# Optimization experiments

Hardware: AMD Instinct MI355X
Metric: run time of the kernel (lower is better)

Reference implementation:

```python
import jax, jax.numpy as jnp
import numpy as np

VAR0, VAR1 = 0.1, 0.2
THRESH = 0.5
NEG_POS = 3
NEG_INF = -1e30


def point_form(b):
    # (cx,cy,w,h) -> (x1,y1,x2,y2)
    return jnp.concatenate([b[..., :2] - b[..., 2:] * 0.5,
                            b[..., :2] + b[..., 2:] * 0.5], -1)


def iou(a, b):
    # a: [G,4], b: [A,4], both xyxy -> [G,A]
    tl = jnp.maximum(a[:, None, :2], b[None, :, :2])
    br = jnp.minimum(a[:, None, 2:], b[None, :, 2:])
    wh = jnp.clip(br - tl, 0.0)
    inter = wh[..., 0] * wh[..., 1]
    area_a = (a[:, 2] - a[:, 0]) * (a[:, 3] - a[:, 1])
    area_b = (b[:, 2] - b[:, 0]) * (b[:, 3] - b[:, 1])
    return inter / (area_a[:, None] + area_b[None, :] - inter)


def encode_single(gt_boxes, gt_labels, anchors):
    # gt_boxes [G,4] xyxy, gt_labels [G], anchors [A,4] cxcywh
    ov = iou(gt_boxes, point_form(anchors))            # [G,A]
    best_prior_idx = jnp.argmax(ov, axis=1)            # [G] guaranteed match
    best_truth_ov = jnp.max(ov, axis=0)                # [A]
    best_truth_idx = jnp.argmax(ov, axis=0)            # [A]
    G = gt_boxes.shape[0]
    best_truth_ov = best_truth_ov.at[best_prior_idx].set(2.0)
    best_truth_idx = best_truth_idx.at[best_prior_idx].set(jnp.arange(G))
    matches = gt_boxes[best_truth_idx]                 # [A,4]
    conf = jnp.where(best_truth_ov < THRESH, 0, gt_labels[best_truth_idx] + 1)
    m_cxcy = (matches[:, :2] + matches[:, 2:]) * 0.5
    m_wh = matches[:, 2:] - matches[:, :2]
    g_cxcy = (m_cxcy - anchors[:, :2]) / (VAR0 * anchors[:, 2:])
    g_wh = jnp.log(m_wh / anchors[:, 2:]) / VAR1
    return conf, jnp.concatenate([g_cxcy, g_wh], -1)


def smooth_l1(d):
    ad = jnp.abs(d)
    return jnp.where(ad < 1.0, 0.5 * d * d, ad - 0.5)


def ssd_guarantee_loss(pred_conf, pred_loc, anchors_b, gt_boxes, gt_labels):
    # anchors_b: per-image anchors [B,A,4] (cxcywh)
    conf_t, loc_t = jax.vmap(encode_single)(gt_boxes, gt_labels, anchors_b)
    loc_t = jax.lax.stop_gradient(loc_t)               # loc_t.detach() in torch
    pos = conf_t > 0                                   # [B,A]
    N = jnp.sum(pos).astype(pred_loc.dtype)
    loc_loss = jnp.sum(jnp.where(pos[..., None], smooth_l1(pred_loc - loc_t), 0.0))
    logp = jax.nn.log_softmax(pred_conf, axis=-1)
    ce = -jnp.take_along_axis(logp, conf_t[..., None], axis=-1)[..., 0]  # [B,A]
    A = pred_conf.shape[1]
    pos_num = jnp.sum(pos, axis=1)                     # [B]
    neg_num = jnp.maximum(10, jnp.minimum(pos_num * NEG_POS, A - pos_num))
    neg_ce = jnp.where(conf_t == 0, ce, NEG_INF)
    neg_sorted = -jnp.sort(-neg_ce, axis=1)            # descending hard-negative sort
    rank = jnp.arange(A)
    take = (rank[None, :] < neg_num[:, None]) & (neg_sorted > 0.5 * NEG_INF)
    class_loss = (jnp.sum(jnp.where(pos, ce, 0.0))
                  + jnp.sum(jnp.where(take, neg_sorted, 0.0))) / N
    return class_loss, loc_loss / N, N


def decode(loc, anchors):
    # loc [B,A,4], anchors [A,4] cxcywh -> refined anchors [B,A,4] cxcywh
    cxcy = anchors[None, :, :2] + loc[..., :2] * VAR0 * anchors[None, :, 2:]
    wh = anchors[None, :, 2:] * jnp.exp(loc[..., 2:] * VAR1)
    return jnp.concatenate([cxcy, wh], -1)


def setup_inputs() -> dict:
    key = jax.random.key(0)
    ks = jax.random.split(key, 10)
    B, A, C, G = 32, 16320, 81, 32
    objectness = jax.random.normal(ks[0], (B, A, 2), jnp.float32)
    refine_loc = 0.1 * jax.random.normal(ks[1], (B, A, 4), jnp.float32)
    pred_conf = jax.random.normal(ks[2], (B, A, C), jnp.float32)
    pred_loc = 0.1 * jax.random.normal(ks[3], (B, A, 4), jnp.float32)
    # anchors: valid normalized cxcywh
    a_cxcy = 0.05 + 0.9 * jax.random.uniform(ks[4], (1, A, 2), jnp.float32)
    a_wh = 0.02 + 0.23 * jax.random.uniform(ks[5], (1, A, 2), jnp.float32)
    anchors = jnp.concatenate([a_cxcy, a_wh], -1)
    # gt boxes: valid xyxy in [0,1]
    g_cxcy = 0.2 + 0.6 * jax.random.uniform(ks[6], (B, G, 2), jnp.float32)
    g_wh = 0.05 + 0.25 * jax.random.uniform(ks[7], (B, G, 2), jnp.float32)
    gt_boxes = jnp.clip(jnp.concatenate([g_cxcy - g_wh * 0.5, g_cxcy + g_wh * 0.5], -1), 0.0, 1.0)
    gt_labels = jax.random.randint(ks[8], (B, G), 0, C - 1, jnp.int32)
    return {"objectness": objectness, "refine_loc": refine_loc, "pred_conf": pred_conf,
            "pred_loc": pred_loc, "anchors": anchors, "gt_boxes": gt_boxes,
            "gt_labels": gt_labels}


def reference(objectness, refine_loc, pred_conf, pred_loc, anchors, gt_boxes, gt_labels):
    a0 = anchors[0]                                    # [A,4]
    B = pred_conf.shape[0]
    anchors_b = jnp.broadcast_to(a0, (B,) + a0.shape)
    # ARM: binary objectness, labels zeroed
    arm_cls, arm_loc, _ = ssd_guarantee_loss(objectness, refine_loc, anchors_b,
                                             gt_boxes, jnp.zeros_like(gt_labels))
    # ODM: match against per-image refined anchors
    refined = decode(refine_loc, a0)
    odm_cls, odm_loc, _ = ssd_guarantee_loss(pred_conf, pred_loc, refined,
                                             gt_boxes, gt_labels)
    total = arm_cls + arm_loc + odm_cls + odm_loc
    return (total, odm_cls, odm_loc, arm_cls, arm_loc)
```

## Files before the change

### kernel.cpp

```cpp
#include <hip/hip_runtime.h>
#include <hip/hip_bf16.h>

constexpr int NB = 32;
constexpr int NA = 16320;
constexpr int NG = 32;
constexpr int NC = 81;
constexpr int ODM_GRID = 2048;

__device__ __forceinline__ float sl1(float d) {
    float ad = fabsf(d);
    return ad < 1.f ? 0.5f * d * d : ad - 0.5f;
}

__device__ __forceinline__ unsigned long long umax64(unsigned long long a, unsigned long long b) {
    return a > b ? a : b;
}

__global__ __launch_bounds__(256) void k_match(
    const float* __restrict__ anchors,
    const float* __restrict__ refine_loc,
    const float* __restrict__ gt_boxes,
    float* __restrict__ ws_ov,
    unsigned char* __restrict__ ws_idx,
    unsigned long long* __restrict__ ws_part)
{
    int row = blockIdx.x >> 6;
    int chunk = blockIdx.x & 63;
    int lossId = row >> 5, b = row & 31;
    int tid = threadIdx.x;
    __shared__ float4 s_gt[NG];
    __shared__ float s_ga[NG];
    __shared__ unsigned long long s_part[4][NG];
    if (tid < NG) {
        float4 g = *(const float4*)&gt_boxes[(size_t)(b * NG + tid) * 4];
        s_gt[tid] = g;
        s_ga[tid] = (g.z - g.x) * (g.w - g.y);
    }
    __syncthreads();
    int a = chunk * 256 + tid;
    bool valid = a < NA;
    int al = valid ? a : NA - 1;
    float4 an = *(const float4*)&anchors[(size_t)al * 4];
    float acx = an.x, acy = an.y, aw = an.z, ah = an.w;
    if (lossId) {
        float4 rl = *(const float4*)&refine_loc[((size_t)b * NA + al) * 4];
        acx += rl.x * 0.1f * aw;
        acy += rl.y * 0.1f * ah;
        aw *= __expf(rl.z * 0.2f);
        ah *= __expf(rl.w * 0.2f);
    }
    float ax1 = acx - aw * 0.5f, ay1 = acy - ah * 0.5f;
    float ax2 = acx + aw * 0.5f, ay2 = acy + ah * 0.5f;
    float aarea = (ax2 - ax1) * (ay2 - ay1);

    float ovg[NG];
    float best = -1.f; int bg = 0;
    #pragma unroll
    for (int g = 0; g < NG; g++) {
        float4 G = s_gt[g];
        float tlx = fmaxf(G.x, ax1);
        float tly = fmaxf(G.y, ay1);
        float brx = fminf(G.z, ax2);
        float bry = fminf(G.w, ay2);
        float w = brx - tlx; w = w > 0.f ? w : 0.f;
        float h = bry - tly; h = h > 0.f ? h : 0.f;
        float inter = w * h;
        float uni = s_ga[g] + aarea - inter;
        float ov = inter * __builtin_amdgcn_rcpf(uni);
        if (!valid) ov = 0.f;
        ovg[g] = ov;
        if (ov > best) { best = ov; bg = g; }
    }
    if (valid) {
        size_t sec = (size_t)row * NA;
        ws_ov[sec + a] = best;
        ws_idx[sec + a] = (unsigned char)bg;
    }
    int lane = tid & 63, wv = tid >> 6;
    #pragma unroll
    for (int g = 0; g < NG; g++) {
        float m = ovg[g];
        m = fmaxf(m, __shfl_xor(m, 1));
        m = fmaxf(m, __shfl_xor(m, 2));
        m = fmaxf(m, __shfl_xor(m, 4));
        m = fmaxf(m, __shfl_xor(m, 8));
        m = fmaxf(m, __shfl_xor(m, 16));
        m = fmaxf(m, __shfl_xor(m, 32));
        unsigned long long ball = __ballot(ovg[g] == m);
        int first = __ffsll((long long)ball) - 1;
        if (lane == 0) {
            unsigned aw_ = (unsigned)(chunk * 256 + wv * 64 + first);
            s_part[wv][g] = ((unsigned long long)__float_as_uint(m) << 32)
                            | (0xFFFFFFFFu - aw_);
        }
    }
    __syncthreads();
    if (tid < NG) {
        unsigned long long k = s_part[0][tid];
        #pragma unroll
        for (int i = 1; i < 4; i++) k = umax64(k, s_part[i][tid]);
        ws_part[(size_t)blockIdx.x * NG + tid] = k;
    }
}

__global__ __launch_bounds__(256) void k_conf(
    const int* __restrict__ gt_labels,
    const unsigned long long* __restrict__ ws_part,
    const float* __restrict__ ws_ov,
    const unsigned char* __restrict__ ws_idx,
    const float* __restrict__ objectness,
    const float* __restrict__ anchors,
    const float* __restrict__ gt_boxes,
    const float* __restrict__ arm_pred,
    int* __restrict__ match,
    float* __restrict__ negce,
    int* __restrict__ pos_cnt,
    float2* __restrict__ pConf)
{
    int row = blockIdx.x >> 3;
    int chunk = blockIdx.x & 7;
    int lossId = row >> 5, b = row & 31;
    int tid = threadIdx.x;
    __shared__ int s_oa[NG];
    __shared__ int s_lab[NG];
    __shared__ float4 s_gt[NG];
    __shared__ unsigned s_mask[512];
    __shared__ unsigned long long s_pp[8][NG];
    for (int i = tid; i < 512; i += 256) s_mask[i] = 0u;
    {
        int g = tid & 31, s = tid >> 5;
        unsigned long long k = 0ull;
        for (int c = s; c < 64; c += 8)
            k = umax64(k, ws_part[(size_t)(row * 64 + c) * NG + g]);
        s_pp[s][g] = k;
    }
    __syncthreads();
    if (tid < NG) {
        unsigned long long k = s_pp[0][tid];
        #pragma unroll
        for (int i = 1; i < 8; i++) k = umax64(k, s_pp[i][tid]);
        unsigned a = 0xFFFFFFFFu - (unsigned)(k & 0xFFFFFFFFull);
        s_oa[tid] = (int)a;
        s_lab[tid] = lossId ? gt_labels[b * NG + tid] : 0;
        s_gt[tid] = *(const float4*)&gt_boxes[(size_t)(b * NG + tid) * 4];
        atomicOr(&s_mask[a >> 5], 1u << (a & 31));
    }
    __syncthreads();
    size_t sec = (size_t)row * NA;
    int base = chunk * 2040;
    int cnt = 0;
    float pce = 0.f, ploc = 0.f;
    for (int a = base + tid; a < base + 2040; a += 256) {
        float ov = ws_ov[sec + a];
        int g = ws_idx[sec + a];
        if (s_mask[a >> 5] & (1u << (a & 31))) {
            for (int j = NG - 1; j >= 0; j--)
                if (s_oa[j] == a) { g = j; ov = 2.0f; break; }
        }
        int conf = (ov < 0.5f) ? 0 : (s_lab[g] + 1);
        cnt += (conf > 0);
        if (lossId) {
            match[sec + a] = conf | (g << 16);
        } else {
            size_t idx = sec + a;
            float2 x = *(const float2*)&objectness[idx * 2];
            float lse = __logf(__expf(x.x) + __expf(x.y));
            float ce = lse - (conf ? x.y : x.x);
            if (conf > 0) {
                pce += ce;
                negce[idx] = 0.f;
                float4 an = *(const float4*)&anchors[(size_t)a * 4];
                float4 G = s_gt[g];
                float mcx = (G.x + G.z) * 0.5f, mcy = (G.y + G.w) * 0.5f;
                float mw = G.z - G.x, mh = G.w - G.y;
                float t0 = (mcx - an.x) / (0.1f * an.z);
                float t1 = (mcy - an.y) / (0.1f * an.w);
                float t2 = __logf(mw / an.z) / 0.2f;
                float t3 = __logf(mh / an.w) / 0.2f;
                float4 pl = *(const float4*)&arm_pred[idx * 4];
                ploc += sl1(pl.x - t0) + sl1(pl.y - t1) + sl1(pl.z - t2) + sl1(pl.w - t3);
            } else {
                negce[idx] = ce;
            }
        }
    }
    #pragma unroll
    for (int o = 32; o > 0; o >>= 1) {
        cnt += __shfl_down(cnt, o);
        pce += __shfl_down(pce, o);
        ploc += __shfl_down(ploc, o);
    }
    __shared__ int s_c[4];
    __shared__ float s_p0[4], s_p1[4];
    if ((tid & 63) == 0) {
        int w = tid >> 6;
        s_c[w] = cnt; s_p0[w] = pce; s_p1[w] = ploc;
    }
    __syncthreads();
    if (tid == 0) {
        pos_cnt[blockIdx.x] = s_c[0] + s_c[1] + s_c[2] + s_c[3];
        pConf[blockIdx.x] = make_float2(s_p0[0] + s_p0[1] + s_p0[2] + s_p0[3],
                                        s_p1[0] + s_p1[1] + s_p1[2] + s_p1[3]);
    }
}

__device__ __forceinline__ void block_reduce2_store(float v0, float v1, float2* dst) {
    #pragma unroll
    for (int o = 32; o > 0; o >>= 1) { v0 += __shfl_down(v0, o); v1 += __shfl_down(v1, o); }
    __shared__ float s0[4], s1[4];
    int w = threadIdx.x >> 6;
    if ((threadIdx.x & 63) == 0) { s0[w] = v0; s1[w] = v1; }
    __syncthreads();
    if (threadIdx.x == 0) {
        float t0 = 0.f, t1 = 0.f;
        #pragma unroll
        for (int i = 0; i < 4; i++) { t0 += s0[i]; t1 += s1[i]; }
        *dst = make_float2(t0, t1);
    }
}

__device__ __forceinline__ void odm_anchor(
    int idx, const float* x, float x80, int m, int sub,
    const float* __restrict__ anchors, const float* __restrict__ refine_loc,
    const float* __restrict__ gt_boxes, const float* __restrict__ pred_loc,
    float* __restrict__ negce, float& pce, float& ploc)
{
    int conf = m & 0xFFFF; int g = m >> 16;
    float s = (sub == 0) ? __expf(x80) : 0.f;
    float sel = (sub == 0 && conf == 80) ? x80 : 0.f;
    #pragma unroll
    for (int j = 0; j < 10; j++) {
        s += __expf(x[j]);
        sel += (sub + 8 * j == conf) ? x[j] : 0.f;
    }
    s += __shfl_xor(s, 1);   sel += __shfl_xor(sel, 1);
    s += __shfl_xor(s, 2);   sel += __shfl_xor(sel, 2);
    s += __shfl_xor(s, 4);   sel += __shfl_xor(sel, 4);
    float ce = __logf(s) - sel;
    if (sub == 0) {
        if (conf > 0) {
            pce += ce;
            negce[idx] = 0.f;
            int b = idx / NA, a = idx - b * NA;
            float4 an = *(const float4*)&anchors[(size_t)a * 4];
            float4 rl = *(const float4*)&refine_loc[(size_t)idx * 4];
            float acx = an.x + rl.x * 0.1f * an.z;
            float acy = an.y + rl.y * 0.1f * an.w;
            float aw = an.z * __expf(rl.z * 0.2f);
            float ah = an.w * __expf(rl.w * 0.2f);
            const float* gb = &gt_boxes[(size_t)(b * NG + g) * 4];
            float mcx = (gb[0] + gb[2]) * 0.5f, mcy = (gb[1] + gb[3]) * 0.5f;
            float mw = gb[2] - gb[0], mh = gb[3] - gb[1];
            float t0 = (mcx - acx) / (0.1f * aw);
            float t1 = (mcy - acy) / (0.1f * ah);
            float t2 = __logf(mw / aw) / 0.2f;
            float t3 = __logf(mh / ah) / 0.2f;
            float4 pl = *(const float4*)&pred_loc[(size_t)idx * 4];
            ploc += sl1(pl.x - t0) + sl1(pl.y - t1) + sl1(pl.z - t2) + sl1(pl.w - t3);
        } else {
            negce[idx] = ce;
        }
    }
}

__global__ __launch_bounds__(256, 4) void k_odm_loss(
    const float* __restrict__ pred_conf,
    const float* __restrict__ pred_loc,
    const float* __restrict__ anchors,
    const float* __restrict__ refine_loc,
    const float* __restrict__ gt_boxes,
    const int* __restrict__ match,
    float* __restrict__ negce,
    float2* __restrict__ partial)
{
    int lane = threadIdx.x & 63;
    int sub = lane & 7;
    int grp = lane >> 3;
    int wid = blockIdx.x * 4 + (threadIdx.x >> 6);
    const int NWAVE = ODM_GRID * 4;
    const int TOT = NB * NA / 8;
    float pce = 0.f, ploc = 0.f;

    float x[10], x80; int m, idx;
    {
        idx = wid * 8 + grp;
        const float* p = pred_conf + (size_t)idx * NC;
        #pragma unroll
        for (int j = 0; j < 10; j++) x[j] = p[sub + 8 * j];
        x80 = (sub == 0) ? p[80] : -87.f;
        m = match[idx];
    }
    for (int gi = wid; gi < TOT; gi += NWAVE) {
        float y[10], y80 = -87.f; int my = 0, idxy = 0;
        int nx = gi + NWAVE;
        if (nx < TOT) {
            idxy = nx * 8 + grp;
            const float* p = pred_conf + (size_t)idxy * NC;
            #pragma unroll
            for (int j = 0; j < 10; j++) y[j] = p[sub + 8 * j];
            y80 = (sub == 0) ? p[80] : -87.f;
            my = match[idxy];
        }
        odm_anchor(idx, x, x80, m, sub, anchors, refine_loc, gt_boxes, pred_loc,
                   negce, pce, ploc);
        #pragma unroll
        for (int j = 0; j < 10; j++) x[j] = y[j];
        x80 = y80; m = my; idx = idxy;
    }
    block_reduce2_store(pce, ploc, &partial[blockIdx.x]);
}

__global__ __launch_bounds__(512) void k_topk(
    const float* __restrict__ negce,
    const int* __restrict__ pos_cnt,
    float* __restrict__ topk)
{
    int blk = blockIdx.x;
    int tid = threadIdx.x;
    size_t sec = (size_t)blk * NA;
    float v[32];
    #pragma unroll
    for (int q = 0; q < 32; q++) {
        int i = tid + (q << 9);
        v[q] = (i < NA) ? negce[sec + i] : 0.f;
    }
    __shared__ int s_red[8];
    __shared__ float s_redf[8];
    int p = 0;
    #pragma unroll
    for (int j = 0; j < 8; j++) p += pos_cnt[blk * 8 + j];
    int k = p * 3; if (k > NA - p) k = NA - p; if (k < 10) k = 10;

    unsigned lo = 0u, hi = 0x7F800000u;
    while (lo < hi) {
        unsigned mid = (lo + hi) >> 1;
        float fmid = __uint_as_float(mid);
        int c = 0;
        #pragma unroll
        for (int q = 0; q < 32; q++) c += (v[q] > fmid);
        #pragma unroll
        for (int o = 32; o > 0; o >>= 1) c += __shfl_down(c, o);
        if ((tid & 63) == 0) s_red[tid >> 6] = c;
        __syncthreads();
        int total = 0;
        #pragma unroll
        for (int j = 0; j < 8; j++) total += s_red[j];
        __syncthreads();
        if (total < k) hi = mid; else lo = mid + 1;
    }
    float V = __uint_as_float(lo);
    int c = 0; float sum = 0.f;
    #pragma unroll
    for (int q = 0; q < 32; q++) {
        if (v[q] > V) { c++; sum += v[q]; }
    }
    #pragma unroll
    for (int o = 32; o > 0; o >>= 1) { c += __shfl_down(c, o); sum += __shfl_down(sum, o); }
    if ((tid & 63) == 0) { s_red[tid >> 6] = c; s_redf[tid >> 6] = sum; }
    __syncthreads();
    if (tid == 0) {
        int cg = 0; float sg = 0.f;
        #pragma unroll
        for (int j = 0; j < 8; j++) { cg += s_red[j]; sg += s_redf[j]; }
        topk[blk] = sg + (float)(k - cg) * V;
    }
}

__global__ __launch_bounds__(256) void k_final(
    const float2* __restrict__ pConf, const float2* __restrict__ pOdm,
    const int* __restrict__ pos_cnt, const float* __restrict__ topk,
    float* __restrict__ out)
{
    int tid = threadIdx.x;
    float a0 = 0.f, a1 = 0.f, o0 = 0.f, o1 = 0.f;
    for (int i = tid; i < 512; i += 256) { float2 v = pConf[i]; a0 += v.x; a1 += v.y; }
    for (int i = tid; i < ODM_GRID; i += 256) { float2 v = pOdm[i]; o0 += v.x; o1 += v.y; }
    float n0 = (float)pos_cnt[tid];
    float n1 = (float)pos_cnt[256 + tid];
    float t0 = (tid < NB) ? topk[tid] : 0.f;
    float t1 = (tid < NB) ? topk[NB + tid] : 0.f;
    #pragma unroll
    for (int o = 32; o > 0; o >>= 1) {
        a0 += __shfl_down(a0, o); a1 += __shfl_down(a1, o);
        o0 += __shfl_down(o0, o); o1 += __shfl_down(o1, o);
        n0 += __shfl_down(n0, o); n1 += __shfl_down(n1, o);
        t0 += __shfl_down(t0, o); t1 += __shfl_down(t1, o);
    }
    __shared__ float s[4][8];
    if ((tid & 63) == 0) {
        int w = tid >> 6;
        s[w][0] = a0; s[w][1] = a1; s[w][2] = o0; s[w][3] = o1;
        s[w][4] = n0; s[w][5] = n1; s[w][6] = t0; s[w][7] = t1;
    }
    __syncthreads();
    if (tid == 0) {
        float armce = 0.f, armloc = 0.f, odmce = 0.f, odmloc = 0.f;
        float N0 = 0.f, N1 = 0.f, tk0 = 0.f, tk1 = 0.f;
        #pragma unroll
        for (int i = 0; i < 4; i++) {
            armce += s[i][0]; armloc += s[i][1]; odmce += s[i][2]; odmloc += s[i][3];
            N0 += s[i][4]; N1 += s[i][5]; tk0 += s[i][6]; tk1 += s[i][7];
        }
        float cls0 = (armce + tk0) / N0, loc0 = armloc / N0;
        float cls1 = (odmce + tk1) / N1, loc1 = odmloc / N1;
        out[0] = cls0 + loc0 + cls1 + loc1;
        out[1] = cls1;
        out[2] = loc1;
        out[3] = cls0;
        out[4] = loc0;
    }
}

extern "C" void kernel_launch(void* const* d_in, const int* in_sizes, int n_in,
                              void* d_out, int out_size, void* d_ws, size_t ws_size,
                              hipStream_t stream) {
    const float* objectness = (const float*)d_in[0];
    const float* refine_loc = (const float*)d_in[1];
    const float* pred_conf  = (const float*)d_in[2];
    const float* pred_loc   = (const float*)d_in[3];
    const float* anchors    = (const float*)d_in[4];
    const float* gt_boxes   = (const float*)d_in[5];
    const int*   gt_labels  = (const int*)d_in[6];

    char* w = (char*)d_ws;
    size_t off = 0;
    int* pos_cnt = (int*)(w + off); off += 512 * sizeof(int);
    float* topk = (float*)(w + off); off += 64 * sizeof(float);
    off = (off + 15) & ~(size_t)15;
    float2* pConf = (float2*)(w + off); off += 512 * 8;
    float2* pOdm = (float2*)(w + off); off += (size_t)ODM_GRID * 8;
    unsigned long long* ws_part = (unsigned long long*)(w + off);
    off += (size_t)64 * 64 * NG * 8;
    off = (off + 15) & ~(size_t)15;
    float* ws_ov = (float*)(w + off); off += (size_t)2 * NB * NA * 4;
    unsigned char* ws_idx = (unsigned char*)(w + off); off += (size_t)2 * NB * NA;
    off = (off + 15) & ~(size_t)15;
    int* match = (int*)(w + off); off += (size_t)2 * NB * NA * 4;
    float* negce = (float*)(w + off); off += (size_t)2 * NB * NA * 4;

    k_match<<<64 * 64, 256, 0, stream>>>(anchors, refine_loc, gt_boxes,
                                         ws_ov, ws_idx, ws_part);
    k_conf<<<64 * 8, 256, 0, stream>>>(gt_labels, ws_part, ws_ov, ws_idx,
                                       objectness, anchors, gt_boxes, refine_loc,
                                       match, negce, pos_cnt, pConf);
    k_odm_loss<<<ODM_GRID, 256, 0, stream>>>(pred_conf, pred_loc, anchors, refine_loc,
                                             gt_boxes, match + (size_t)NB * NA,
                                             negce + (size_t)NB * NA, pOdm);
    k_topk<<<2 * NB, 512, 0, stream>>>(negce, pos_cnt, topk);
    k_final<<<1, 256, 0, stream>>>(pConf, pOdm, pos_cnt, topk, (float*)d_out);
}
```

Baseline: 131.1 us.

## Fuse final reduction into topk via last-block counter and deepen ODM prefetch

```diff
diff --git a/kernel.cpp b/kernel.cpp
--- a/kernel.cpp
+++ b/kernel.cpp
@@ -115,8 +115,10 @@
     int* __restrict__ match,
     float* __restrict__ negce,
     int* __restrict__ pos_cnt,
-    float2* __restrict__ pConf)
+    float2* __restrict__ pConf,
+    unsigned* __restrict__ done_cnt)
 {
+    if (blockIdx.x == 0 && threadIdx.x == 0) *done_cnt = 0u;
     int row = blockIdx.x >> 3;
     int chunk = blockIdx.x & 7;
     int lossId = row >> 5, b = row & 31;
@@ -220,14 +222,14 @@
 }
 
 __device__ __forceinline__ void odm_anchor(
-    int idx, const float* x, float x80, int m, int sub,
+    int idx, const float* x, int m, int sub,
     const float* __restrict__ anchors, const float* __restrict__ refine_loc,
     const float* __restrict__ gt_boxes, const float* __restrict__ pred_loc,
     float* __restrict__ negce, float& pce, float& ploc)
 {
     int conf = m & 0xFFFF; int g = m >> 16;
-    float s = (sub == 0) ? __expf(x80) : 0.f;
-    float sel = (sub == 0 && conf == 80) ? x80 : 0.f;
+    float s = (sub == 0) ? __expf(x[10]) : 0.f;
+    float sel = (sub == 0 && conf == 80) ? x[10] : 0.f;
     #pragma unroll
     for (int j = 0; j < 10; j++) {
         s += __expf(x[j]);
@@ -277,35 +279,39 @@
     int sub = lane & 7;
     int grp = lane >> 3;
     int wid = blockIdx.x * 4 + (threadIdx.x >> 6);
-    const int NWAVE = ODM_GRID * 4;
     const int TOT = NB * NA / 8;
     float pce = 0.f, ploc = 0.f;
 
-    float x[10], x80; int m, idx;
-    {
-        idx = wid * 8 + grp;
-        const float* p = pred_conf + (size_t)idx * NC;
+    float xA[2][11], xB[2][11];
+    int mA[2], mB[2], idA[2], idB[2];
+
+    auto LOAD = [&](float (&x)[11], int& m, int& id, int group) {
+        id = group * 8 + grp;
+        const float* p = pred_conf + (size_t)id * NC;
         #pragma unroll
         for (int j = 0; j < 10; j++) x[j] = p[sub + 8 * j];
-        x80 = (sub == 0) ? p[80] : -87.f;
-        m = match[idx];
-    }
-    for (int gi = wid; gi < TOT; gi += NWAVE) {
-        float y[10], y80 = -87.f; int my = 0, idxy = 0;
-        int nx = gi + NWAVE;
-        if (nx < TOT) {
-            idxy = nx * 8 + grp;
-            const float* p = pred_conf + (size_t)idxy * NC;
-            #pragma unroll
-            for (int j = 0; j < 10; j++) y[j] = p[sub + 8 * j];
-            y80 = (sub == 0) ? p[80] : -87.f;
-            my = match[idxy];
-        }
-        odm_anchor(idx, x, x80, m, sub, anchors, refine_loc, gt_boxes, pred_loc,
-                   negce, pce, ploc);
-        #pragma unroll
-        for (int j = 0; j < 10; j++) x[j] = y[j];
-        x80 = y80; m = my; idx = idxy;
+        x[10] = (sub == 0) ? p[80] : -87.f;
+        m = match[id];
+    };
+
+    bool bLast = (wid + 8192 + 3 * 16384) < TOT;
+    LOAD(xA[0], mA[0], idA[0], wid);
+    LOAD(xB[0], mB[0], idB[0], wid + 8192);
+    #pragma unroll
+    for (int k = 0; k < 4; k++) {
+        int cur = k & 1, nxt = cur ^ 1;
+        if (k < 3)
+            LOAD(xA[nxt], mA[nxt], idA[nxt], wid + (k + 1) * 16384);
+        odm_anchor(idA[cur], xA[cur], mA[cur], sub, anchors, refine_loc, gt_boxes,
+                   pred_loc, negce, pce, ploc);
+        if (k < 3) {
+            int gB = wid + 8192 + (k + 1) * 16384;
+            if (k + 1 < 3 || bLast)
+                LOAD(xB[nxt], mB[nxt], idB[nxt], gB);
+        }
+        if (k < 3 || bLast)
+            odm_anchor(idB[cur], xB[cur], mB[cur], sub, anchors, refine_loc, gt_boxes,
+                       pred_loc, negce, pce, ploc);
     }
     block_reduce2_store(pce, ploc, &partial[blockIdx.x]);
 }
@@ -313,7 +319,11 @@
 __global__ __launch_bounds__(512) void k_topk(
     const float* __restrict__ negce,
     const int* __restrict__ pos_cnt,
-    float* __restrict__ topk)
+    const float2* __restrict__ pConf,
+    const float2* __restrict__ pOdm,
+    float* __restrict__ topk,
+    unsigned* __restrict__ done_cnt,
+    float* __restrict__ out)
 {
     int blk = blockIdx.x;
     int tid = threadIdx.x;
@@ -364,19 +374,18 @@
         for (int j = 0; j < 8; j++) { cg += s_red[j]; sg += s_redf[j]; }
         topk[blk] = sg + (float)(k - cg) * V;
     }
-}
-
-__global__ __launch_bounds__(256) void k_final(
-    const float2* __restrict__ pConf, const float2* __restrict__ pOdm,
-    const int* __restrict__ pos_cnt, const float* __restrict__ topk,
-    float* __restrict__ out)
-{
-    int tid = threadIdx.x;
+    __threadfence();
+    __shared__ unsigned s_t;
+    if (tid == 0) s_t = atomicAdd(done_cnt, 1u);
+    __syncthreads();
+    if (s_t != 2 * NB - 1) return;
+
     float a0 = 0.f, a1 = 0.f, o0 = 0.f, o1 = 0.f;
-    for (int i = tid; i < 512; i += 256) { float2 v = pConf[i]; a0 += v.x; a1 += v.y; }
-    for (int i = tid; i < ODM_GRID; i += 256) { float2 v = pOdm[i]; o0 += v.x; o1 += v.y; }
-    float n0 = (float)pos_cnt[tid];
-    float n1 = (float)pos_cnt[256 + tid];
+    { float2 vv = pConf[tid]; a0 += vv.x; a1 += vv.y; }
+    #pragma unroll
+    for (int i = 0; i < 4; i++) { float2 vv = pOdm[tid + i * 512]; o0 += vv.x; o1 += vv.y; }
+    float n0 = (tid < 256) ? (float)pos_cnt[tid] : 0.f;
+    float n1 = (tid < 256) ? (float)pos_cnt[256 + tid] : 0.f;
     float t0 = (tid < NB) ? topk[tid] : 0.f;
     float t1 = (tid < NB) ? topk[NB + tid] : 0.f;
     #pragma unroll
@@ -386,7 +395,7 @@
         n0 += __shfl_down(n0, o); n1 += __shfl_down(n1, o);
         t0 += __shfl_down(t0, o); t1 += __shfl_down(t1, o);
     }
-    __shared__ float s[4][8];
+    __shared__ float s[8][8];
     if ((tid & 63) == 0) {
         int w = tid >> 6;
         s[w][0] = a0; s[w][1] = a1; s[w][2] = o0; s[w][3] = o1;
@@ -397,7 +406,7 @@
         float armce = 0.f, armloc = 0.f, odmce = 0.f, odmloc = 0.f;
         float N0 = 0.f, N1 = 0.f, tk0 = 0.f, tk1 = 0.f;
         #pragma unroll
-        for (int i = 0; i < 4; i++) {
+        for (int i = 0; i < 8; i++) {
             armce += s[i][0]; armloc += s[i][1]; odmce += s[i][2]; odmloc += s[i][3];
             N0 += s[i][4]; N1 += s[i][5]; tk0 += s[i][6]; tk1 += s[i][7];
         }
@@ -426,6 +435,7 @@
     size_t off = 0;
     int* pos_cnt = (int*)(w + off); off += 512 * sizeof(int);
     float* topk = (float*)(w + off); off += 64 * sizeof(float);
+    unsigned* done_cnt = (unsigned*)(w + off); off += 16;
     off = (off + 15) & ~(size_t)15;
     float2* pConf = (float2*)(w + off); off += 512 * 8;
     float2* pOdm = (float2*)(w + off); off += (size_t)ODM_GRID * 8;
@@ -442,10 +452,10 @@
                                          ws_ov, ws_idx, ws_part);
     k_conf<<<64 * 8, 256, 0, stream>>>(gt_labels, ws_part, ws_ov, ws_idx,
                                        objectness, anchors, gt_boxes, refine_loc,
-                                       match, negce, pos_cnt, pConf);
+                                       match, negce, pos_cnt, pConf, done_cnt);
     k_odm_loss<<<ODM_GRID, 256, 0, stream>>>(pred_conf, pred_loc, anchors, refine_loc,
                                              gt_boxes, match + (size_t)NB * NA,
                                              negce + (size_t)NB * NA, pOdm);
-    k_topk<<<2 * NB, 512, 0, stream>>>(negce, pos_cnt, topk);
-    k_final<<<1, 256, 0, stream>>>(pConf, pOdm, pos_cnt, topk, (float*)d_out);
-}
+    k_topk<<<2 * NB, 512, 0, stream>>>(negce, pos_cnt, pConf, pOdm, topk, done_cnt,
+                                       (float*)d_out);
+}
```

Result: slower. 135.3 us (+3.2%).

## Stream ODM confidence rows into LDS with triple-buffered async global loads

Applied to the files above, without the earlier changes.

```diff
diff --git a/kernel.cpp b/kernel.cpp
--- a/kernel.cpp
+++ b/kernel.cpp
@@ -5,7 +5,10 @@
 constexpr int NA = 16320;
 constexpr int NG = 32;
 constexpr int NC = 81;
-constexpr int ODM_GRID = 2048;
+constexpr int ODM_GRID = 2040;
+
+#define AS1 __attribute__((address_space(1)))
+#define AS3 __attribute__((address_space(3)))
 
 __device__ __forceinline__ float sl1(float d) {
     float ad = fabsf(d);
@@ -219,51 +222,7 @@
     }
 }
 
-__device__ __forceinline__ void odm_anchor(
-    int idx, const float* x, float x80, int m, int sub,
-    const float* __restrict__ anchors, const float* __restrict__ refine_loc,
-    const float* __restrict__ gt_boxes, const float* __restrict__ pred_loc,
-    float* __restrict__ negce, float& pce, float& ploc)
-{
-    int conf = m & 0xFFFF; int g = m >> 16;
-    float s = (sub == 0) ? __expf(x80) : 0.f;
-    float sel = (sub == 0 && conf == 80) ? x80 : 0.f;
-    #pragma unroll
-    for (int j = 0; j < 10; j++) {
-        s += __expf(x[j]);
-        sel += (sub + 8 * j == conf) ? x[j] : 0.f;
-    }
-    s += __shfl_xor(s, 1);   sel += __shfl_xor(sel, 1);
-    s += __shfl_xor(s, 2);   sel += __shfl_xor(sel, 2);
-    s += __shfl_xor(s, 4);   sel += __shfl_xor(sel, 4);
-    float ce = __logf(s) - sel;
-    if (sub == 0) {
-        if (conf > 0) {
-            pce += ce;
-            negce[idx] = 0.f;
-            int b = idx / NA, a = idx - b * NA;
-            float4 an = *(const float4*)&anchors[(size_t)a * 4];
-            float4 rl = *(const float4*)&refine_loc[(size_t)idx * 4];
-            float acx = an.x + rl.x * 0.1f * an.z;
-            float acy = an.y + rl.y * 0.1f * an.w;
-            float aw = an.z * __expf(rl.z * 0.2f);
-            float ah = an.w * __expf(rl.w * 0.2f);
-            const float* gb = &gt_boxes[(size_t)(b * NG + g) * 4];
-            float mcx = (gb[0] + gb[2]) * 0.5f, mcy = (gb[1] + gb[3]) * 0.5f;
-            float mw = gb[2] - gb[0], mh = gb[3] - gb[1];
-            float t0 = (mcx - acx) / (0.1f * aw);
-            float t1 = (mcy - acy) / (0.1f * ah);
-            float t2 = __logf(mw / aw) / 0.2f;
-            float t3 = __logf(mh / ah) / 0.2f;
-            float4 pl = *(const float4*)&pred_loc[(size_t)idx * 4];
-            ploc += sl1(pl.x - t0) + sl1(pl.y - t1) + sl1(pl.z - t2) + sl1(pl.w - t3);
-        } else {
-            negce[idx] = ce;
-        }
-    }
-}
-
-__global__ __launch_bounds__(256, 4) void k_odm_loss(
+__global__ __launch_bounds__(256) void k_odm_loss(
     const float* __restrict__ pred_conf,
     const float* __restrict__ pred_loc,
     const float* __restrict__ anchors,
@@ -273,39 +232,92 @@
     float* __restrict__ negce,
     float2* __restrict__ partial)
 {
-    int lane = threadIdx.x & 63;
+    __shared__ unsigned sbuf[4][3][656];
+    int tid = threadIdx.x;
+    int lane = tid & 63;
+    int wv = tid >> 6;
     int sub = lane & 7;
     int grp = lane >> 3;
-    int wid = blockIdx.x * 4 + (threadIdx.x >> 6);
-    const int NWAVE = ODM_GRID * 4;
-    const int TOT = NB * NA / 8;
+    int wid = blockIdx.x * 4 + wv;
+    int tbase = wid * 8;
     float pce = 0.f, ploc = 0.f;
 
-    float x[10], x80; int m, idx;
-    {
-        idx = wid * 8 + grp;
-        const float* p = pred_conf + (size_t)idx * NC;
-        #pragma unroll
-        for (int j = 0; j < 10; j++) x[j] = p[sub + 8 * j];
-        x80 = (sub == 0) ? p[80] : -87.f;
-        m = match[idx];
-    }
-    for (int gi = wid; gi < TOT; gi += NWAVE) {
-        float y[10], y80 = -87.f; int my = 0, idxy = 0;
-        int nx = gi + NWAVE;
-        if (nx < TOT) {
-            idxy = nx * 8 + grp;
-            const float* p = pred_conf + (size_t)idxy * NC;
-            #pragma unroll
-            for (int j = 0; j < 10; j++) y[j] = p[sub + 8 * j];
-            y80 = (sub == 0) ? p[80] : -87.f;
-            my = match[idxy];
-        }
-        odm_anchor(idx, x, x80, m, sub, anchors, refine_loc, gt_boxes, pred_loc,
-                   negce, pce, ploc);
-        #pragma unroll
-        for (int j = 0; j < 10; j++) x[j] = y[j];
-        x80 = y80; m = my; idx = idxy;
+    const AS1 unsigned* gconf = (const AS1 unsigned*)pred_conf;
+    const AS1 unsigned* gmatch = (const AS1 unsigned*)match;
+
+    auto STAGE = [&](int t) {
+        int b3 = t % 3;
+        size_t gi = (size_t)(tbase + t);
+        const AS1 unsigned* gp = gconf + gi * 648;
+        __builtin_amdgcn_global_load_lds((const AS1 void*)(gp + lane * 4),
+                                         (AS3 void*)&sbuf[wv][b3][0], 16, 0, 0);
+        __builtin_amdgcn_global_load_lds((const AS1 void*)(gp + 256 + lane * 4),
+                                         (AS3 void*)&sbuf[wv][b3][256], 16, 0, 0);
+        if (lane < 34)
+            __builtin_amdgcn_global_load_lds((const AS1 void*)(gp + 512 + lane * 4),
+                                             (AS3 void*)&sbuf[wv][b3][512], 16, 0, 0);
+        if (lane < 8)
+            __builtin_amdgcn_global_load_lds((const AS1 void*)(gmatch + gi * 8 + lane),
+                                             (AS3 void*)&sbuf[wv][b3][648], 4, 0, 0);
+    };
+
+    auto COMPUTE = [&](int i) {
+        int b3 = i % 3;
+        int gi = tbase + i;
+        int idx = gi * 8 + grp;
+        const unsigned* sb = &sbuf[wv][b3][0];
+        float x[11];
+        #pragma unroll
+        for (int j = 0; j < 10; j++) x[j] = __uint_as_float(sb[grp * 81 + sub + 8 * j]);
+        x[10] = (sub == 0) ? __uint_as_float(sb[grp * 81 + 80]) : -87.f;
+        int m = (int)sb[648 + grp];
+        int conf = m & 0xFFFF; int g = m >> 16;
+        float s = __expf(x[10]);
+        float sel = (sub == 0 && conf == 80) ? x[10] : 0.f;
+        #pragma unroll
+        for (int j = 0; j < 10; j++) {
+            s += __expf(x[j]);
+            sel += (sub + 8 * j == conf) ? x[j] : 0.f;
+        }
+        s += __shfl_xor(s, 1);   sel += __shfl_xor(sel, 1);
+        s += __shfl_xor(s, 2);   sel += __shfl_xor(sel, 2);
+        s += __shfl_xor(s, 4);   sel += __shfl_xor(sel, 4);
+        float ce = __logf(s) - sel;
+        if (sub == 0) {
+            if (conf > 0) {
+                pce += ce;
+                negce[idx] = 0.f;
+                int b = idx / NA, a = idx - b * NA;
+                float4 an = *(const float4*)&anchors[(size_t)a * 4];
+                float4 rl = *(const float4*)&refine_loc[(size_t)idx * 4];
+                float acx = an.x + rl.x * 0.1f * an.z;
+                float acy = an.y + rl.y * 0.1f * an.w;
+                float aw = an.z * __expf(rl.z * 0.2f);
+                float ah = an.w * __expf(rl.w * 0.2f);
+                const float* gb = &gt_boxes[(size_t)(b * NG + g) * 4];
+                float mcx = (gb[0] + gb[2]) * 0.5f, mcy = (gb[1] + gb[3]) * 0.5f;
+                float mw = gb[2] - gb[0], mh = gb[3] - gb[1];
+                float t0 = (mcx - acx) / (0.1f * aw);
+                float t1 = (mcy - acy) / (0.1f * ah);
+                float t2 = __logf(mw / aw) / 0.2f;
+                float t3 = __logf(mh / ah) / 0.2f;
+                float4 pl = *(const float4*)&pred_loc[(size_t)idx * 4];
+                ploc += sl1(pl.x - t0) + sl1(pl.y - t1) + sl1(pl.z - t2) + sl1(pl.w - t3);
+            } else {
+                negce[idx] = ce;
+            }
+        }
+    };
+
+    STAGE(0);
+    STAGE(1);
+    #pragma unroll
+    for (int i = 0; i < 8; i++) {
+        if (i == 0)      asm volatile("s_waitcnt vmcnt(4)" ::: "memory");
+        else if (i == 7) asm volatile("s_waitcnt vmcnt(1)" ::: "memory");
+        else             asm volatile("s_waitcnt vmcnt(5)" ::: "memory");
+        if (i < 6) STAGE(i + 2);
+        COMPUTE(i);
     }
     block_reduce2_store(pce, ploc, &partial[blockIdx.x]);
 }
```

Result: no change. 131.7 us (+0.5%).

## Overlap ODM log-sum-exp with matching in a fused kernel; split CE gather

Applied to the files above, without the earlier changes.

```diff
diff --git a/kernel.cpp b/kernel.cpp
--- a/kernel.cpp
+++ b/kernel.cpp
@@ -5,7 +5,8 @@
 constexpr int NA = 16320;
 constexpr int NG = 32;
 constexpr int NC = 81;
-constexpr int ODM_GRID = 2048;
+constexpr int LSE_BLKS = 2048;
+constexpr int CE_BLKS = 2040;
 
 __device__ __forceinline__ float sl1(float d) {
     float ad = fabsf(d);
@@ -16,21 +17,67 @@
     return a > b ? a : b;
 }
 
-__global__ __launch_bounds__(256) void k_match(
+__global__ __launch_bounds__(256) void k_mega(
     const float* __restrict__ anchors,
     const float* __restrict__ refine_loc,
     const float* __restrict__ gt_boxes,
+    const float* __restrict__ pred_conf,
+    float* __restrict__ lse,
     float* __restrict__ ws_ov,
     unsigned char* __restrict__ ws_idx,
     unsigned long long* __restrict__ ws_part)
 {
-    int row = blockIdx.x >> 6;
-    int chunk = blockIdx.x & 63;
-    int lossId = row >> 5, b = row & 31;
-    int tid = threadIdx.x;
     __shared__ float4 s_gt[NG];
     __shared__ float s_ga[NG];
     __shared__ unsigned long long s_part[4][NG];
+
+    int bid = blockIdx.x;
+    int q = bid / 3, r3 = bid - q * 3;
+    int tid = threadIdx.x;
+
+    if (r3 == 0) {
+        int lane = tid & 63, sub = lane & 7, grp = lane >> 3;
+        int wid = q * 4 + (tid >> 6);
+        const int NWAVE = LSE_BLKS * 4;
+        const int TOT = NB * NA / 8;
+        float x[11]; int idx;
+        {
+            idx = wid * 8 + grp;
+            const float* p = pred_conf + (size_t)idx * NC;
+            #pragma unroll
+            for (int j = 0; j < 10; j++) x[j] = p[sub + 8 * j];
+            x[10] = (sub == 0) ? p[80] : -87.f;
+        }
+        for (int gi = wid; gi < TOT; gi += NWAVE) {
+            float y[11]; int idy = 0;
+            int nx = gi + NWAVE;
+            if (nx < TOT) {
+                idy = nx * 8 + grp;
+                const float* p = pred_conf + (size_t)idy * NC;
+                #pragma unroll
+                for (int j = 0; j < 10; j++) y[j] = p[sub + 8 * j];
+                y[10] = (sub == 0) ? p[80] : -87.f;
+            } else {
+                #pragma unroll
+                for (int j = 0; j < 11; j++) y[j] = -87.f;
+            }
+            float s = __expf(x[10]);
+            #pragma unroll
+            for (int j = 0; j < 10; j++) s += __expf(x[j]);
+            s += __shfl_xor(s, 1);
+            s += __shfl_xor(s, 2);
+            s += __shfl_xor(s, 4);
+            if (sub == 0) lse[idx] = __logf(s);
+            #pragma unroll
+            for (int j = 0; j < 11; j++) x[j] = y[j];
+            idx = idy;
+        }
+        return;
+    }
+
+    int mb = 2 * q + (r3 - 1);
+    int row = mb >> 6, chunk = mb & 63;
+    int lossId = row >> 5, b = row & 31;
     if (tid < NG) {
         float4 g = *(const float4*)&gt_boxes[(size_t)(b * NG + tid) * 4];
         s_gt[tid] = g;
@@ -53,9 +100,9 @@
     float ax2 = acx + aw * 0.5f, ay2 = acy + ah * 0.5f;
     float aarea = (ax2 - ax1) * (ay2 - ay1);
 
-    float ovg[NG];
+    int lane = tid & 63, wv = tid >> 6;
     float best = -1.f; int bg = 0;
-    #pragma unroll
+    #pragma unroll 1
     for (int g = 0; g < NG; g++) {
         float4 G = s_gt[g];
         float tlx = fmaxf(G.x, ax1);
@@ -65,28 +112,17 @@
         float w = brx - tlx; w = w > 0.f ? w : 0.f;
         float h = bry - tly; h = h > 0.f ? h : 0.f;
         float inter = w * h;
-        float uni = s_ga[g] + aarea - inter;
-        float ov = inter * __builtin_amdgcn_rcpf(uni);
+        float ov = inter * __builtin_amdgcn_rcpf(s_ga[g] + aarea - inter);
         if (!valid) ov = 0.f;
-        ovg[g] = ov;
         if (ov > best) { best = ov; bg = g; }
-    }
-    if (valid) {
-        size_t sec = (size_t)row * NA;
-        ws_ov[sec + a] = best;
-        ws_idx[sec + a] = (unsigned char)bg;
-    }
-    int lane = tid & 63, wv = tid >> 6;
-    #pragma unroll
-    for (int g = 0; g < NG; g++) {
-        float m = ovg[g];
+        float m = ov;
         m = fmaxf(m, __shfl_xor(m, 1));
         m = fmaxf(m, __shfl_xor(m, 2));
         m = fmaxf(m, __shfl_xor(m, 4));
         m = fmaxf(m, __shfl_xor(m, 8));
         m = fmaxf(m, __shfl_xor(m, 16));
         m = fmaxf(m, __shfl_xor(m, 32));
-        unsigned long long ball = __ballot(ovg[g] == m);
+        unsigned long long ball = __ballot(ov == m);
         int first = __ffsll((long long)ball) - 1;
         if (lane == 0) {
             unsigned aw_ = (unsigned)(chunk * 256 + wv * 64 + first);
@@ -94,12 +130,17 @@
                             | (0xFFFFFFFFu - aw_);
         }
     }
+    if (valid) {
+        size_t sec = (size_t)row * NA;
+        ws_ov[sec + a] = best;
+        ws_idx[sec + a] = (unsigned char)bg;
+    }
     __syncthreads();
     if (tid < NG) {
         unsigned long long k = s_part[0][tid];
         #pragma unroll
         for (int i = 1; i < 4; i++) k = umax64(k, s_part[i][tid]);
-        ws_part[(size_t)blockIdx.x * NG + tid] = k;
+        ws_part[(size_t)mb * NG + tid] = k;
     }
 }
 
@@ -164,8 +205,8 @@
         } else {
             size_t idx = sec + a;
             float2 x = *(const float2*)&objectness[idx * 2];
-            float lse = __logf(__expf(x.x) + __expf(x.y));
-            float ce = lse - (conf ? x.y : x.x);
+            float lse2 = __logf(__expf(x.x) + __expf(x.y));
+            float ce = lse2 - (conf ? x.y : x.x);
             if (conf > 0) {
                 pce += ce;
                 negce[idx] = 0.f;
@@ -204,110 +245,58 @@
     }
 }
 
-__device__ __forceinline__ void block_reduce2_store(float v0, float v1, float2* dst) {
-    #pragma unroll
-    for (int o = 32; o > 0; o >>= 1) { v0 += __shfl_down(v0, o); v1 += __shfl_down(v1, o); }
-    __shared__ float s0[4], s1[4];
-    int w = threadIdx.x >> 6;
-    if ((threadIdx.x & 63) == 0) { s0[w] = v0; s1[w] = v1; }
-    __syncthreads();
-    if (threadIdx.x == 0) {
-        float t0 = 0.f, t1 = 0.f;
-        #pragma unroll
-        for (int i = 0; i < 4; i++) { t0 += s0[i]; t1 += s1[i]; }
-        *dst = make_float2(t0, t1);
-    }
-}
-
-__device__ __forceinline__ void odm_anchor(
-    int idx, const float* x, float x80, int m, int sub,
-    const float* __restrict__ anchors, const float* __restrict__ refine_loc,
-    const float* __restrict__ gt_boxes, const float* __restrict__ pred_loc,
-    float* __restrict__ negce, float& pce, float& ploc)
-{
-    int conf = m & 0xFFFF; int g = m >> 16;
-    float s = (sub == 0) ? __expf(x80) : 0.f;
-    float sel = (sub == 0 && conf == 80) ? x80 : 0.f;
-    #pragma unroll
-    for (int j = 0; j < 10; j++) {
-        s += __expf(x[j]);
-        sel += (sub + 8 * j == conf) ? x[j] : 0.f;
-    }
-    s += __shfl_xor(s, 1);   sel += __shfl_xor(sel, 1);
-    s += __shfl_xor(s, 2);   sel += __shfl_xor(sel, 2);
-    s += __shfl_xor(s, 4);   sel += __shfl_xor(sel, 4);
-    float ce = __logf(s) - sel;
-    if (sub == 0) {
-        if (conf > 0) {
-            pce += ce;
-            negce[idx] = 0.f;
-            int b = idx / NA, a = idx - b * NA;
-            float4 an = *(const float4*)&anchors[(size_t)a * 4];
-            float4 rl = *(const float4*)&refine_loc[(size_t)idx * 4];
-            float acx = an.x + rl.x * 0.1f * an.z;
-            float acy = an.y + rl.y * 0.1f * an.w;
-            float aw = an.z * __expf(rl.z * 0.2f);
-            float ah = an.w * __expf(rl.w * 0.2f);
-            const float* gb = &gt_boxes[(size_t)(b * NG + g) * 4];
-            float mcx = (gb[0] + gb[2]) * 0.5f, mcy = (gb[1] + gb[3]) * 0.5f;
-            float mw = gb[2] - gb[0], mh = gb[3] - gb[1];
-            float t0 = (mcx - acx) / (0.1f * aw);
-            float t1 = (mcy - acy) / (0.1f * ah);
-            float t2 = __logf(mw / aw) / 0.2f;
-            float t3 = __logf(mh / ah) / 0.2f;
-            float4 pl = *(const float4*)&pred_loc[(size_t)idx * 4];
-            ploc += sl1(pl.x - t0) + sl1(pl.y - t1) + sl1(pl.z - t2) + sl1(pl.w - t3);
-        } else {
-            negce[idx] = ce;
-        }
-    }
-}
-
-__global__ __launch_bounds__(256, 4) void k_odm_loss(
+__global__ __launch_bounds__(256) void k_ce(
     const float* __restrict__ pred_conf,
     const float* __restrict__ pred_loc,
     const float* __restrict__ anchors,
     const float* __restrict__ refine_loc,
     const float* __restrict__ gt_boxes,
     const int* __restrict__ match,
+    const float* __restrict__ lse,
     float* __restrict__ negce,
     float2* __restrict__ partial)
 {
-    int lane = threadIdx.x & 63;
-    int sub = lane & 7;
-    int grp = lane >> 3;
-    int wid = blockIdx.x * 4 + (threadIdx.x >> 6);
-    const int NWAVE = ODM_GRID * 4;
-    const int TOT = NB * NA / 8;
+    int idx = blockIdx.x * 256 + threadIdx.x;
+    int m = match[idx];
+    int conf = m & 0xFFFF; int g = m >> 16;
+    float xc = pred_conf[(size_t)idx * NC + conf];
+    float ce = lse[idx] - xc;
     float pce = 0.f, ploc = 0.f;
-
-    float x[10], x80; int m, idx;
-    {
-        idx = wid * 8 + grp;
-        const float* p = pred_conf + (size_t)idx * NC;
-        #pragma unroll
-        for (int j = 0; j < 10; j++) x[j] = p[sub + 8 * j];
-        x80 = (sub == 0) ? p[80] : -87.f;
-        m = match[idx];
-    }
-    for (int gi = wid; gi < TOT; gi += NWAVE) {
-        float y[10], y80 = -87.f; int my = 0, idxy = 0;
-        int nx = gi + NWAVE;
-        if (nx < TOT) {
-            idxy = nx * 8 + grp;
-            const float* p = pred_conf + (size_t)idxy * NC;
-            #pragma unroll
-            for (int j = 0; j < 10; j++) y[j] = p[sub + 8 * j];
-            y80 = (sub == 0) ? p[80] : -87.f;
-            my = match[idxy];
-        }
-        odm_anchor(idx, x, x80, m, sub, anchors, refine_loc, gt_boxes, pred_loc,
-                   negce, pce, ploc);
-        #pragma unroll
-        for (int j = 0; j < 10; j++) x[j] = y[j];
-        x80 = y80; m = my; idx = idxy;
-    }
-    block_reduce2_store(pce, ploc, &partial[blockIdx.x]);
+    if (conf > 0) {
+        pce = ce;
+        negce[idx] = 0.f;
+        int b = idx / NA, a = idx - b * NA;
+        float4 an = *(const float4*)&anchors[(size_t)a * 4];
+        float4 rl = *(const float4*)&refine_loc[(size_t)idx * 4];
+        float acx = an.x + rl.x * 0.1f * an.z;
+        float acy = an.y + rl.y * 0.1f * an.w;
+        float aw = an.z * __expf(rl.z * 0.2f);
+        float ah = an.w * __expf(rl.w * 0.2f);
+        const float* gb = &gt_boxes[(size_t)(b * NG + g) * 4];
+        float mcx = (gb[0] + gb[2]) * 0.5f, mcy = (gb[1] + gb[3]) * 0.5f;
+        float mw = gb[2] - gb[0], mh = gb[3] - gb[1];
+        float t0 = (mcx - acx) / (0.1f * aw);
+        float t1 = (mcy - acy) / (0.1f * ah);
+        float t2 = __logf(mw / aw) / 0.2f;
+        float t3 = __logf(mh / ah) / 0.2f;
+        float4 pl = *(const float4*)&pred_loc[(size_t)idx * 4];
+        ploc = sl1(pl.x - t0) + sl1(pl.y - t1) + sl1(pl.z - t2) + sl1(pl.w - t3);
+    } else {
+        negce[idx] = ce;
+    }
+    #pragma unroll
+    for (int o = 32; o > 0; o >>= 1) {
+        pce += __shfl_down(pce, o);
+        ploc += __shfl_down(ploc, o);
+    }
+    __shared__ float s0[4], s1[4];
+    int w = threadIdx.x >> 6;
+    if ((threadIdx.x & 63) == 0) { s0[w] = pce; s1[w] = ploc; }
+    __syncthreads();
+    if (threadIdx.x == 0) {
+        partial[blockIdx.x] = make_float2(s0[0] + s0[1] + s0[2] + s0[3],
+                                          s1[0] + s1[1] + s1[2] + s1[3]);
+    }
 }
 
 __global__ __launch_bounds__(512) void k_topk(
@@ -374,7 +363,7 @@
     int tid = threadIdx.x;
     float a0 = 0.f, a1 = 0.f, o0 = 0.f, o1 = 0.f;
     for (int i = tid; i < 512; i += 256) { float2 v = pConf[i]; a0 += v.x; a1 += v.y; }
-    for (int i = tid; i < ODM_GRID; i += 256) { float2 v = pOdm[i]; o0 += v.x; o1 += v.y; }
+    for (int i = tid; i < CE_BLKS; i += 256) { float2 v = pOdm[i]; o0 += v.x; o1 += v.y; }
     float n0 = (float)pos_cnt[tid];
     float n1 = (float)pos_cnt[256 + tid];
     float t0 = (tid < NB) ? topk[tid] : 0.f;
@@ -428,24 +417,25 @@
     float* topk = (float*)(w + off); off += 64 * sizeof(float);
     off = (off + 15) & ~(size_t)15;
     float2* pConf = (float2*)(w + off); off += 512 * 8;
-    float2* pOdm = (float2*)(w + off); off += (size_t)ODM_GRID * 8;
+    float2* pOdm = (float2*)(w + off); off += (size_t)CE_BLKS * 8;
     unsigned long long* ws_part = (unsigned long long*)(w + off);
-    off += (size_t)64 * 64 * NG * 8;
+    off += (size_t)4096 * NG * 8;
     off = (off + 15) & ~(size_t)15;
+    float* lse = (float*)(w + off); off += (size_t)NB * NA * 4;
     float* ws_ov = (float*)(w + off); off += (size_t)2 * NB * NA * 4;
     unsigned char* ws_idx = (unsigned char*)(w + off); off += (size_t)2 * NB * NA;
     off = (off + 15) & ~(size_t)15;
     int* match = (int*)(w + off); off += (size_t)2 * NB * NA * 4;
     float* negce = (float*)(w + off); off += (size_t)2 * NB * NA * 4;
 
-    k_match<<<64 * 64, 256, 0, stream>>>(anchors, refine_loc, gt_boxes,
-                                         ws_ov, ws_idx, ws_part);
+    k_mega<<<3 * 2048, 256, 0, stream>>>(anchors, refine_loc, gt_boxes, pred_conf,
+                                         lse, ws_ov, ws_idx, ws_part);
     k_conf<<<64 * 8, 256, 0, stream>>>(gt_labels, ws_part, ws_ov, ws_idx,
                                        objectness, anchors, gt_boxes, refine_loc,
                                        match, negce, pos_cnt, pConf);
-    k_odm_loss<<<ODM_GRID, 256, 0, stream>>>(pred_conf, pred_loc, anchors, refine_loc,
-                                             gt_boxes, match + (size_t)NB * NA,
-                                             negce + (size_t)NB * NA, pOdm);
+    k_ce<<<CE_BLKS, 256, 0, stream>>>(pred_conf, pred_loc, anchors, refine_loc, gt_boxes,
+                                      match + (size_t)NB * NA, lse,
+                                      negce + (size_t)NB * NA, pOdm);
     k_topk<<<2 * NB, 512, 0, stream>>>(negce, pos_cnt, topk);
     k_final<<<1, 256, 0, stream>>>(pConf, pOdm, pos_cnt, topk, (float*)d_out);
 }
```

After: 121.2 us (median of 2 runs). -7.5%, faster.
